# Optimization experiments

Measured on AMD Instinct MI355X. Metric: run time of the kernel, lower is better.

Reference implementation:

```python
import jax, jax.numpy as jnp
import numpy as np

EPS = 1e-12  # matches tf.nn.l2_normalize epsilon used by keras backend


def l2n(x, axis):
    return x / jnp.sqrt(jnp.maximum(jnp.sum(x * x, axis=axis, keepdims=True), EPS))


def setup_inputs() -> dict:
    key = jax.random.key(0)
    k1, k2, k3 = jax.random.split(key, 3)
    B, T, D, P = 32, 256, 512, 20
    inp_a = jax.random.normal(k1, (B, T, D), dtype=jnp.float32)
    inp_b = jax.random.normal(k2, (B, T, D), dtype=jnp.float32)
    # build(): output_dim weights of shape (1, D), 'uniform' init -> stacked (P, D)
    W = jax.random.uniform(k3, (P, D), dtype=jnp.float32, minval=-0.05, maxval=0.05)
    return {"inp_a": inp_a, "inp_b": inp_b, "W": W}


def reference(inp_a, inp_b, W):
    # l2-normalize over feature dim
    na = l2n(inp_a, -1)  # (B,T,D)
    nb = l2n(inp_b, -1)  # (B,T,D)
    # K.batch_dot(outp_b, outp_a, axes=[1,1]): contract seq axis -> (B,D,D)
    alpha = jnp.einsum('btd,bte->bde', nb, na)
    alpha = l2n(alpha, 1)
    # K.batch_dot(outp_b, alpha, axes=[2,1]): contract feature axis of b with axis1 of alpha -> (B,T,D)
    hmean = jnp.einsum('btd,bde->bte', nb, alpha)
    # per-perspective weighting + l2-normalize, vectorized over P perspectives
    aw = l2n(inp_a[:, :, None, :] * W[None, None, :, :], -1)   # (B,T,P,D)
    hw = l2n(hmean[:, :, None, :] * W[None, None, :, :], -1)   # (B,T,P,D)
    # batch_dot(hw_i, aw_i, axes=[2,2]) * eye summed == rowwise dot (diagonal only)
    persp = jnp.sum(aw * hw, axis=-1)  # (B,T,P)
    return (persp, persp)
```

## Files before the change

kernel.cpp:

```cpp
#include <hip/hip_runtime.h>
#include <hip/hip_bf16.h>

#define BB 32
#define TT 256
#define DD 512
#define PP 20
#define EPSF 1e-12f
#define BTP (BB * TT * PP)

typedef __attribute__((ext_vector_type(8))) short short8;
typedef __attribute__((ext_vector_type(4))) float f32x4;

__device__ inline unsigned short f2bf(float f) {
    unsigned u = __float_as_uint(f);
    u += 0x7fffu + ((u >> 16) & 1u);
    return (unsigned short)(u >> 16);
}
__device__ inline unsigned pk2(float lo, float hi) {
    __hip_bfloat162 h = __float22bfloat162_rn(float2{lo, hi});
    union { __hip_bfloat162 h; unsigned u; } c;
    c.h = h;
    return c.u;
}
__device__ inline float bf2f(unsigned s) {
    return __uint_as_float(s << 16);
}

union U8 { short8 s; uint4 u; };

__global__ __launch_bounds__(256)
void k_prep(const float* __restrict__ a, const float* __restrict__ b,
            const float* __restrict__ W,
            unsigned short* __restrict__ na_bf,
            unsigned short* __restrict__ nb_bf,
            float* __restrict__ q, unsigned short* __restrict__ W2) {
    const int row  = blockIdx.x * 4 + (threadIdx.x >> 6);
    const int lane = threadIdx.x & 63;
    const float4* pa = (const float4*)(a + (size_t)row * DD);
    const float4* pb = (const float4*)(b + (size_t)row * DD);
    float4 a0 = pa[2 * lane], a1 = pa[2 * lane + 1];
    float4 b0 = pb[2 * lane], b1 = pb[2 * lane + 1];
    float sa = a0.x * a0.x + a0.y * a0.y + a0.z * a0.z + a0.w * a0.w
             + a1.x * a1.x + a1.y * a1.y + a1.z * a1.z + a1.w * a1.w;
    float sb = b0.x * b0.x + b0.y * b0.y + b0.z * b0.z + b0.w * b0.w
             + b1.x * b1.x + b1.y * b1.y + b1.z * b1.z + b1.w * b1.w;
#pragma unroll
    for (int off = 1; off < 64; off <<= 1) {
        sa += __shfl_xor(sa, off);
        sb += __shfl_xor(sb, off);
    }
    const float ia_ = rsqrtf(fmaxf(sa, EPSF));
    const float ib_ = rsqrtf(fmaxf(sb, EPSF));
    uint4 oa, ob;
    oa.x = pk2(a0.x * ia_, a0.y * ia_);
    oa.y = pk2(a0.z * ia_, a0.w * ia_);
    oa.z = pk2(a1.x * ia_, a1.y * ia_);
    oa.w = pk2(a1.z * ia_, a1.w * ia_);
    ob.x = pk2(b0.x * ib_, b0.y * ib_);
    ob.y = pk2(b0.z * ib_, b0.w * ib_);
    ob.z = pk2(b1.x * ib_, b1.y * ib_);
    ob.w = pk2(b1.z * ib_, b1.w * ib_);
    *(uint4*)(na_bf + (size_t)row * DD + 8 * lane) = oa;
    *(uint4*)(nb_bf + (size_t)row * DD + 8 * lane) = ob;
    if (lane < 2) {
        const int i2 = 2 * row + lane;
        q[i2] = 0.f;
        const float w = (i2 < PP * DD) ? W[i2] : 0.f;
        W2[i2] = f2bf(w * w);
    }
}

__global__ __launch_bounds__(256)
void k_gemm_g(const unsigned short* __restrict__ nb,
              unsigned short* __restrict__ G) {
    const int bz  = blockIdx.z;
    const int tid = threadIdx.x;
    const int t0 = blockIdx.y * 64;
    const int s0 = blockIdx.x * 64;
    __shared__ __align__(16) unsigned short As[64 * 72];
    __shared__ __align__(16) unsigned short Bs[64 * 72];

    const int wave = tid >> 6, lane = tid & 63;
    const int quad = lane >> 4, ln = lane & 15;
    const int wm = wave >> 1, wn = wave & 1;

    const unsigned short* nbb = nb + (size_t)bz * TT * DD;

    const int lr  = tid >> 2;
    const int c16 = (tid & 3) * 16;

    f32x4 acc[2][2];
#pragma unroll
    for (int i = 0; i < 2; ++i)
#pragma unroll
        for (int j = 0; j < 2; ++j)
#pragma unroll
            for (int r = 0; r < 4; ++r) acc[i][j][r] = 0.f;

    uint4 pa0 = *(const uint4*)(nbb + (size_t)(t0 + lr) * DD + c16);
    uint4 pa1 = *(const uint4*)(nbb + (size_t)(t0 + lr) * DD + c16 + 8);
    uint4 pb0 = *(const uint4*)(nbb + (size_t)(s0 + lr) * DD + c16);
    uint4 pb1 = *(const uint4*)(nbb + (size_t)(s0 + lr) * DD + c16 + 8);

    for (int k0 = 0; k0 < DD; k0 += 64) {
        *(uint4*)&As[lr * 72 + c16]     = pa0;
        *(uint4*)&As[lr * 72 + c16 + 8] = pa1;
        *(uint4*)&Bs[lr * 72 + c16]     = pb0;
        *(uint4*)&Bs[lr * 72 + c16 + 8] = pb1;
        if (k0 + 64 < DD) {
            pa0 = *(const uint4*)(nbb + (size_t)(t0 + lr) * DD + k0 + 64 + c16);
            pa1 = *(const uint4*)(nbb + (size_t)(t0 + lr) * DD + k0 + 64 + c16 + 8);
            pb0 = *(const uint4*)(nbb + (size_t)(s0 + lr) * DD + k0 + 64 + c16);
            pb1 = *(const uint4*)(nbb + (size_t)(s0 + lr) * DD + k0 + 64 + c16 + 8);
        }
        __syncthreads();
        short8 af[2][2], bfr[2][2];
#pragma unroll
        for (int h = 0; h < 2; ++h) {
            af[h][0]  = *(const short8*)&As[(wm * 32 + ln) * 72 + h * 32 + quad * 8];
            af[h][1]  = *(const short8*)&As[(wm * 32 + 16 + ln) * 72 + h * 32 + quad * 8];
            bfr[h][0] = *(const short8*)&Bs[(wn * 32 + ln) * 72 + h * 32 + quad * 8];
            bfr[h][1] = *(const short8*)&Bs[(wn * 32 + 16 + ln) * 72 + h * 32 + quad * 8];
        }
#pragma unroll
        for (int h = 0; h < 2; ++h)
#pragma unroll
            for (int i = 0; i < 2; ++i)
#pragma unroll
                for (int j = 0; j < 2; ++j)
                    acc[i][j] = __builtin_amdgcn_mfma_f32_16x16x32_bf16(
                        af[h][i], bfr[h][j], acc[i][j], 0, 0, 0);
        __syncthreads();
    }
    unsigned short* Gb = G + (size_t)bz * TT * TT;
#pragma unroll
    for (int i = 0; i < 2; ++i)
#pragma unroll
        for (int j = 0; j < 2; ++j) {
            const int col = s0 + wn * 32 + j * 16 + ln;
            const int row0 = t0 + wm * 32 + i * 16 + quad * 4;
#pragma unroll
            for (int r = 0; r < 4; r += 2) {
                const unsigned pk = pk2(acc[i][j][r], acc[i][j][r + 1]);
                Gb[(size_t)(row0 + r) * TT + col] = (unsigned short)pk;
                Gb[(size_t)(row0 + r + 1) * TT + col] = (unsigned short)(pk >> 16);
            }
        }
}

__global__ __launch_bounds__(256, 4)
void k_gemm_h(const unsigned short* __restrict__ G,
              const unsigned short* __restrict__ na,
              unsigned short* __restrict__ H, float* __restrict__ q) {
    const int bz = blockIdx.z;
    const int t0 = blockIdx.y * 64;
    const int e0 = blockIdx.x * 64;
    __shared__ __align__(16) unsigned short AB[2 * 64 * 40];
    __shared__ float qsum[64];
    unsigned short* As = AB;
    unsigned short* Bs = AB + 64 * 40;

    const int tid  = threadIdx.x;
    const int wave = tid >> 6, lane = tid & 63;
    const int quad = lane >> 4, ln = lane & 15;
    const int wm = wave >> 1, wn = wave & 1;

    const unsigned short* Gb  = G  + (size_t)bz * TT * TT;
    const unsigned short* nab = na + (size_t)bz * TT * DD;

    const int lr = tid >> 2;
    const int c8 = (tid & 3) * 8;
    const int eglow = tid & 3;
    const int spair = (tid >> 2) & 15;
    const int eg    = eglow + 4 * (tid >> 6);

    f32x4 acc[2][2];
#pragma unroll
    for (int i = 0; i < 2; ++i)
#pragma unroll
        for (int j = 0; j < 2; ++j)
#pragma unroll
            for (int r = 0; r < 4; ++r) acc[i][j][r] = 0.f;

    uint4 pga = *(const uint4*)(Gb + (size_t)(t0 + lr) * TT + c8);
    uint4 cva, cvb;
    if (tid < 128) {
        cva = *(const uint4*)(nab + (size_t)(2 * spair) * DD + e0 + eg * 8);
        cvb = *(const uint4*)(nab + (size_t)(2 * spair + 1) * DD + e0 + eg * 8);
    }

    unsigned* bp = (unsigned*)Bs;
    for (int k0 = 0; k0 < TT; k0 += 32) {
        *(uint4*)&As[lr * 40 + c8] = pga;
        if (tid < 128) {
            const int base = eg * 160 + spair;
            unsigned lo, hi;
            lo = cva.x; hi = cvb.x;
            bp[base +   0] = (lo & 0xffffu) | (hi << 16);
            bp[base +  20] = (lo >> 16) | (hi & 0xffff0000u);
            lo = cva.y; hi = cvb.y;
            bp[base +  40] = (lo & 0xffffu) | (hi << 16);
            bp[base +  60] = (lo >> 16) | (hi & 0xffff0000u);
            lo = cva.z; hi = cvb.z;
            bp[base +  80] = (lo & 0xffffu) | (hi << 16);
            bp[base + 100] = (lo >> 16) | (hi & 0xffff0000u);
            lo = cva.w; hi = cvb.w;
            bp[base + 120] = (lo & 0xffffu) | (hi << 16);
            bp[base + 140] = (lo >> 16) | (hi & 0xffff0000u);
        }
        if (k0 + 32 < TT) {
            pga = *(const uint4*)(Gb + (size_t)(t0 + lr) * TT + k0 + 32 + c8);
            if (tid < 128) {
                cva = *(const uint4*)(nab + (size_t)(k0 + 32 + 2 * spair) * DD + e0 + eg * 8);
                cvb = *(const uint4*)(nab + (size_t)(k0 + 32 + 2 * spair + 1) * DD + e0 + eg * 8);
            }
        }
        __syncthreads();
        short8 af[2], bfr[2];
        af[0]  = *(const short8*)&As[(wm * 32 + ln) * 40 + quad * 8];
        af[1]  = *(const short8*)&As[(wm * 32 + 16 + ln) * 40 + quad * 8];
        bfr[0] = *(const short8*)&Bs[(wn * 32 + ln) * 40 + quad * 8];
        bfr[1] = *(const short8*)&Bs[(wn * 32 + 16 + ln) * 40 + quad * 8];
#pragma unroll
        for (int i = 0; i < 2; ++i)
#pragma unroll
            for (int j = 0; j < 2; ++j)
                acc[i][j] = __builtin_amdgcn_mfma_f32_16x16x32_bf16(
                    af[i], bfr[j], acc[i][j], 0, 0, 0);
        __syncthreads();
    }

    unsigned short* Ns = AB;
    {
        const int r0_ = tid >> 3, k8 = (tid & 7) * 8;
        *(uint4*)&Ns[r0_ * 72 + k8] =
            *(const uint4*)(nab + (size_t)(t0 + r0_) * DD + e0 + k8);
        const int c1 = tid + 256;
        const int r1_ = c1 >> 3, k8b = (c1 & 7) * 8;
        *(uint4*)&Ns[r1_ * 72 + k8b] =
            *(const uint4*)(nab + (size_t)(t0 + r1_) * DD + e0 + k8b);
    }
    if (tid < 64) qsum[tid] = 0.f;
    __syncthreads();

    unsigned short* Hb = H + (size_t)bz * TT * DD;
#pragma unroll
    for (int j = 0; j < 2; ++j) {
        const int col  = e0 + wn * 32 + j * 16 + ln;
        const int lcol = wn * 32 + j * 16 + ln;
        float qp = 0.f;
#pragma unroll
        for (int i = 0; i < 2; ++i) {
            const int row0  = t0 + wm * 32 + i * 16 + quad * 4;
            const int lrow0 = wm * 32 + i * 16 + quad * 4;
#pragma unroll
            for (int r = 0; r < 4; r += 2) {
                const float hv0 = acc[i][j][r];
                const float hv1 = acc[i][j][r + 1];
                const unsigned pk = pk2(hv0, hv1);
                Hb[(size_t)(row0 + r) * DD + col] = (unsigned short)pk;
                Hb[(size_t)(row0 + r + 1) * DD + col] = (unsigned short)(pk >> 16);
                qp = fmaf(bf2f(Ns[(lrow0 + r) * 72 + lcol]), hv0, qp);
                qp = fmaf(bf2f(Ns[(lrow0 + r + 1) * 72 + lcol]), hv1, qp);
            }
        }
        qp += __shfl_xor(qp, 16);
        qp += __shfl_xor(qp, 32);
        if (quad == 0) atomicAdd(&qsum[wn * 32 + j * 16 + ln], qp);
    }
    __syncthreads();
    if (tid < 64) atomicAdd(q + bz * DD + e0 + tid, qsum[tid]);
}

__global__ __launch_bounds__(256)
void k_persp_mfma(const unsigned short* __restrict__ na,
                  const unsigned short* __restrict__ H,
                  const float* __restrict__ q,
                  const unsigned short* __restrict__ W2,
                  float* __restrict__ out) {
    const int b    = blockIdx.y;
    const int r0   = blockIdx.x * 16;
    const int wave = threadIdx.x >> 6;
    const int lane = threadIdx.x & 63;
    const int quad = lane >> 4, ln = lane & 15;
    const size_t rowbase = ((size_t)b * TT + r0 + ln) * DD;

    __shared__ float qs[DD];
    __shared__ float ps[3][64][24];
    {
        const float* qb = q + (size_t)b * DD;
        float2 v = *(const float2*)(qb + 2 * threadIdx.x);
        qs[2 * threadIdx.x + 0] = rsqrtf(fmaxf(v.x, EPSF));
        qs[2 * threadIdx.x + 1] = rsqrtf(fmaxf(v.y, EPSF));
    }
    __syncthreads();

    f32x4 s1[2], s2[2], s3[2];
#pragma unroll
    for (int j = 0; j < 2; ++j)
#pragma unroll
        for (int r = 0; r < 4; ++r) { s1[j][r] = 0.f; s2[j][r] = 0.f; s3[j][r] = 0.f; }

    const int kbeg = wave * 128;
#pragma unroll
    for (int ki = 0; ki < 4; ++ki) {
        const int k0 = kbeg + ki * 32;
        const int k = k0 + quad * 8;
        uint4 au = *(const uint4*)(na + rowbase + k);
        uint4 hu = *(const uint4*)(H + rowbase + k);
        float4 q0 = *(const float4*)&qs[k];
        float4 q1 = *(const float4*)&qs[k + 4];
        const float av[8] = {bf2f(au.x & 0xffffu), bf2f(au.x >> 16),
                             bf2f(au.y & 0xffffu), bf2f(au.y >> 16),
                             bf2f(au.z & 0xffffu), bf2f(au.z >> 16),
                             bf2f(au.w & 0xffffu), bf2f(au.w >> 16)};
        const float qv[8] = {q0.x, q0.y, q0.z, q0.w, q1.x, q1.y, q1.z, q1.w};
        float hv[8] = {bf2f(hu.x & 0xffffu), bf2f(hu.x >> 16),
                       bf2f(hu.y & 0xffffu), bf2f(hu.y >> 16),
                       bf2f(hu.z & 0xffffu), bf2f(hu.z >> 16),
                       bf2f(hu.w & 0xffffu), bf2f(hu.w >> 16)};
#pragma unroll
        for (int t = 0; t < 8; ++t) hv[t] *= qv[t];
        U8 ah, aa, hh;
        ah.u.x = pk2(av[0] * hv[0], av[1] * hv[1]);
        ah.u.y = pk2(av[2] * hv[2], av[3] * hv[3]);
        ah.u.z = pk2(av[4] * hv[4], av[5] * hv[5]);
        ah.u.w = pk2(av[6] * hv[6], av[7] * hv[7]);
        aa.u.x = pk2(av[0] * av[0], av[1] * av[1]);
        aa.u.y = pk2(av[2] * av[2], av[3] * av[3]);
        aa.u.z = pk2(av[4] * av[4], av[5] * av[5]);
        aa.u.w = pk2(av[6] * av[6], av[7] * av[7]);
        hh.u.x = pk2(hv[0] * hv[0], hv[1] * hv[1]);
        hh.u.y = pk2(hv[2] * hv[2], hv[3] * hv[3]);
        hh.u.z = pk2(hv[4] * hv[4], hv[5] * hv[5]);
        hh.u.w = pk2(hv[6] * hv[6], hv[7] * hv[7]);
        short8 bw0 = *(const short8*)(W2 + (size_t)ln * DD + k);
        short8 bw1 = *(const short8*)(W2 + (size_t)(16 + ln) * DD + k);
        s1[0] = __builtin_amdgcn_mfma_f32_16x16x32_bf16(ah.s, bw0, s1[0], 0, 0, 0);
        s1[1] = __builtin_amdgcn_mfma_f32_16x16x32_bf16(ah.s, bw1, s1[1], 0, 0, 0);
        s2[0] = __builtin_amdgcn_mfma_f32_16x16x32_bf16(aa.s, bw0, s2[0], 0, 0, 0);
        s2[1] = __builtin_amdgcn_mfma_f32_16x16x32_bf16(aa.s, bw1, s2[1], 0, 0, 0);
        s3[0] = __builtin_amdgcn_mfma_f32_16x16x32_bf16(hh.s, bw0, s3[0], 0, 0, 0);
        s3[1] = __builtin_amdgcn_mfma_f32_16x16x32_bf16(hh.s, bw1, s3[1], 0, 0, 0);
    }

    if (wave >= 1) {
#pragma unroll
        for (int j = 0; j < 2; ++j)
#pragma unroll
            for (int r = 0; r < 4; ++r) {
                ps[wave - 1][lane][j * 4 + r]      = s1[j][r];
                ps[wave - 1][lane][8 + j * 4 + r]  = s2[j][r];
                ps[wave - 1][lane][16 + j * 4 + r] = s3[j][r];
            }
    }
    __syncthreads();
    if (wave == 0) {
#pragma unroll
        for (int j = 0; j < 2; ++j) {
            const int p = j * 16 + ln;
            if (p < PP) {
#pragma unroll
                for (int r = 0; r < 4; ++r) {
                    const float v1 = s1[j][r] + ps[0][lane][j * 4 + r]
                                   + ps[1][lane][j * 4 + r] + ps[2][lane][j * 4 + r];
                    const float v2 = s2[j][r] + ps[0][lane][8 + j * 4 + r]
                                   + ps[1][lane][8 + j * 4 + r] + ps[2][lane][8 + j * 4 + r];
                    const float v3 = s3[j][r] + ps[0][lane][16 + j * 4 + r]
                                   + ps[1][lane][16 + j * 4 + r] + ps[2][lane][16 + j * 4 + r];
                    const size_t row = (size_t)b * TT + r0 + quad * 4 + r;
                    const float v = v1 * rsqrtf(fmaxf(v2, EPSF))
                                       * rsqrtf(fmaxf(v3, EPSF));
                    out[row * PP + p] = v;
                    out[(size_t)BTP + row * PP + p] = v;
                }
            }
        }
    }
}

extern "C" void kernel_launch(void* const* d_in, const int* in_sizes, int n_in,
                              void* d_out, int out_size, void* d_ws, size_t ws_size,
                              hipStream_t stream) {
    (void)in_sizes; (void)n_in; (void)out_size; (void)ws_size;
    const float* a = (const float*)d_in[0];
    const float* b = (const float*)d_in[1];
    const float* W = (const float*)d_in[2];
    float* out = (float*)d_out;

    char* ws = (char*)d_ws;
    unsigned short* nb_bf = (unsigned short*)ws;
    unsigned short* na_bf = (unsigned short*)(ws + (8u << 20));
    unsigned short* G_bf  = (unsigned short*)(ws + (16u << 20));
    unsigned short* H_bf  = (unsigned short*)(ws + (20u << 20));
    float* q     = (float*)(ws + (28u << 20));
    unsigned short* W2 = (unsigned short*)(ws + (28u << 20) + (64u << 10));

    k_prep<<<BB * TT / 4, 256, 0, stream>>>(a, b, W, na_bf, nb_bf, q, W2);

    dim3 gG(4, 4, BB);
    k_gemm_g<<<gG, 256, 0, stream>>>(nb_bf, G_bf);

    dim3 gH(DD / 64, TT / 64, BB);
    k_gemm_h<<<gH, 256, 0, stream>>>(G_bf, na_bf, H_bf, q);

    dim3 gP(TT / 16, BB);
    k_persp_mfma<<<gP, 256, 0, stream>>>(na_bf, H_bf, q, W2, out);
}
```

Before: 104.5 us.

## Move inp_a normalization into G-GEMM launch to overlap with GEMM blocks

```diff
diff --git a/kernel.cpp b/kernel.cpp
--- a/kernel.cpp
+++ b/kernel.cpp
@@ -29,38 +29,23 @@
 union U8 { short8 s; uint4 u; };
 
 __global__ __launch_bounds__(256)
-void k_prep(const float* __restrict__ a, const float* __restrict__ b,
-            const float* __restrict__ W,
-            unsigned short* __restrict__ na_bf,
-            unsigned short* __restrict__ nb_bf,
-            float* __restrict__ q, unsigned short* __restrict__ W2) {
+void k_prep_b(const float* __restrict__ b, const float* __restrict__ W,
+              unsigned short* __restrict__ nb_bf,
+              float* __restrict__ q, unsigned short* __restrict__ W2) {
     const int row  = blockIdx.x * 4 + (threadIdx.x >> 6);
     const int lane = threadIdx.x & 63;
-    const float4* pa = (const float4*)(a + (size_t)row * DD);
     const float4* pb = (const float4*)(b + (size_t)row * DD);
-    float4 a0 = pa[2 * lane], a1 = pa[2 * lane + 1];
     float4 b0 = pb[2 * lane], b1 = pb[2 * lane + 1];
-    float sa = a0.x * a0.x + a0.y * a0.y + a0.z * a0.z + a0.w * a0.w
-             + a1.x * a1.x + a1.y * a1.y + a1.z * a1.z + a1.w * a1.w;
     float sb = b0.x * b0.x + b0.y * b0.y + b0.z * b0.z + b0.w * b0.w
              + b1.x * b1.x + b1.y * b1.y + b1.z * b1.z + b1.w * b1.w;
 #pragma unroll
-    for (int off = 1; off < 64; off <<= 1) {
-        sa += __shfl_xor(sa, off);
-        sb += __shfl_xor(sb, off);
-    }
-    const float ia_ = rsqrtf(fmaxf(sa, EPSF));
+    for (int off = 1; off < 64; off <<= 1) sb += __shfl_xor(sb, off);
     const float ib_ = rsqrtf(fmaxf(sb, EPSF));
-    uint4 oa, ob;
-    oa.x = pk2(a0.x * ia_, a0.y * ia_);
-    oa.y = pk2(a0.z * ia_, a0.w * ia_);
-    oa.z = pk2(a1.x * ia_, a1.y * ia_);
-    oa.w = pk2(a1.z * ia_, a1.w * ia_);
+    uint4 ob;
     ob.x = pk2(b0.x * ib_, b0.y * ib_);
     ob.y = pk2(b0.z * ib_, b0.w * ib_);
     ob.z = pk2(b1.x * ib_, b1.y * ib_);
     ob.w = pk2(b1.z * ib_, b1.w * ib_);
-    *(uint4*)(na_bf + (size_t)row * DD + 8 * lane) = oa;
     *(uint4*)(nb_bf + (size_t)row * DD + 8 * lane) = ob;
     if (lane < 2) {
         const int i2 = 2 * row + lane;
@@ -71,16 +56,42 @@
 }
 
 __global__ __launch_bounds__(256)
-void k_gemm_g(const unsigned short* __restrict__ nb,
-              unsigned short* __restrict__ G) {
-    const int bz  = blockIdx.z;
+void k_g_pa(const unsigned short* __restrict__ nb,
+            const float* __restrict__ a,
+            unsigned short* __restrict__ G,
+            unsigned short* __restrict__ na_bf) {
+    const int blk = blockIdx.x;
     const int tid = threadIdx.x;
-    const int t0 = blockIdx.y * 64;
-    const int s0 = blockIdx.x * 64;
+    const int wave = tid >> 6, lane = tid & 63;
+
     __shared__ __align__(16) unsigned short As[64 * 72];
     __shared__ __align__(16) unsigned short Bs[64 * 72];
 
-    const int wave = tid >> 6, lane = tid & 63;
+    if (blk >= 512) {
+        const int idx = blk - 512;
+#pragma unroll 1
+        for (int it = 0; it < 4; ++it) {
+            const int row = idx * 16 + it * 4 + wave;
+            const float4* pa = (const float4*)(a + (size_t)row * DD);
+            float4 a0 = pa[2 * lane], a1 = pa[2 * lane + 1];
+            float sa = a0.x * a0.x + a0.y * a0.y + a0.z * a0.z + a0.w * a0.w
+                     + a1.x * a1.x + a1.y * a1.y + a1.z * a1.z + a1.w * a1.w;
+#pragma unroll
+            for (int off = 1; off < 64; off <<= 1) sa += __shfl_xor(sa, off);
+            const float ia_ = rsqrtf(fmaxf(sa, EPSF));
+            uint4 oa;
+            oa.x = pk2(a0.x * ia_, a0.y * ia_);
+            oa.y = pk2(a0.z * ia_, a0.w * ia_);
+            oa.z = pk2(a1.x * ia_, a1.y * ia_);
+            oa.w = pk2(a1.z * ia_, a1.w * ia_);
+            *(uint4*)(na_bf + (size_t)row * DD + 8 * lane) = oa;
+        }
+        return;
+    }
+
+    const int bz = blk >> 4;
+    const int t0 = ((blk >> 2) & 3) * 64;
+    const int s0 = (blk & 3) * 64;
     const int quad = lane >> 4, ln = lane & 15;
     const int wm = wave >> 1, wn = wave & 1;
 
@@ -396,10 +407,9 @@
     float* q     = (float*)(ws + (28u << 20));
     unsigned short* W2 = (unsigned short*)(ws + (28u << 20) + (64u << 10));
 
-    k_prep<<<BB * TT / 4, 256, 0, stream>>>(a, b, W, na_bf, nb_bf, q, W2);
-
-    dim3 gG(4, 4, BB);
-    k_gemm_g<<<gG, 256, 0, stream>>>(nb_bf, G_bf);
+    k_prep_b<<<BB * TT / 4, 256, 0, stream>>>(b, W, nb_bf, q, W2);
+
+    k_g_pa<<<1024, 256, 0, stream>>>(nb_bf, a, G_bf, na_bf);
 
     dim3 gH(DD / 64, TT / 64, BB);
     k_gemm_h<<<gH, 256, 0, stream>>>(G_bf, na_bf, H_bf, q);
```

Result: no change. 104.1 us (-0.4%).
